# Optimization experiments

Measured on AMD Instinct MI355X. Metric: run time of the kernel, lower is better.

Reference implementation:

```python
import jax, jax.numpy as jnp
import numpy as np
from jax import lax

N_G, E_G, E_LG = 100000, 400000, 1200000
N_T, E_T, E_LGT = 50000, 100000, 300000
D_F, D_MSG_G = 64, 128
VOCAB, D_EMB, D_MSG_T = 780, 128, 128
N_ITERS_G, N_ITERS_T = 4, 4
SCALE = 0.05  # keep relu/sum chains numerically tame over iterations


def setup_inputs() -> dict:
    key = jax.random.key(0)
    ks = jax.random.split(key, 32)
    f32 = jnp.float32
    w = lambda k, sh: jax.random.normal(k, sh, f32) * SCALE
    return {
        "G_f": jax.random.normal(ks[0], (N_G, D_F), f32),
        "G_ef": jax.random.normal(ks[1], (E_G, D_F), f32),
        "G_src": jax.random.randint(ks[2], (E_G,), 0, N_G, jnp.int32),
        "G_dst": jax.random.randint(ks[3], (E_G,), 0, N_G, jnp.int32),
        "G_lg_src": jax.random.randint(ks[4], (E_LG,), 0, E_G, jnp.int32),
        "G_lg_dst": jax.random.randint(ks[5], (E_LG,), 0, E_G, jnp.int32),
        "T_id": jax.random.randint(ks[6], (N_T,), 0, VOCAB, jnp.int32),
        "T_src": jax.random.randint(ks[7], (E_T,), 0, N_T, jnp.int32),
        "T_dst": jax.random.randint(ks[8], (E_T,), 0, N_T, jnp.int32),
        "T_lg_src": jax.random.randint(ks[9], (E_LGT,), 0, E_T, jnp.int32),
        "T_lg_dst": jax.random.randint(ks[10], (E_LGT,), 0, E_T, jnp.int32),
        "embeddings": jax.random.normal(ks[11], (VOCAB, D_EMB), f32),
        "W1": w(ks[12], (D_F, D_MSG_G)),
        "W2": w(ks[13], (D_F, D_MSG_G)),
        "W3": w(ks[14], (D_MSG_G, D_MSG_G)),
        "U1_G": w(ks[15], (D_F, D_MSG_G)),
        "U2_G": w(ks[16], (D_MSG_G, D_MSG_G)),
        "Wz": w(ks[17], (D_EMB, D_MSG_T)),
        "Uz": w(ks[18], (D_MSG_T, D_MSG_T)),
        "Wr": w(ks[19], (D_EMB, D_MSG_T)),
        "Ur": w(ks[20], (D_MSG_T, D_MSG_T)),
        "Wh": w(ks[21], (D_EMB, D_MSG_T)),
        "Uh": w(ks[22], (D_MSG_T, D_MSG_T)),
        "U1_T": w(ks[23], (D_EMB, D_MSG_T)),
        "U2_T": w(ks[24], (D_MSG_T, D_MSG_T)),
    }


def reference(G_f, G_ef, G_src, G_dst, G_lg_src, G_lg_dst,
              T_id, T_src, T_dst, T_lg_src, T_lg_dst,
              embeddings, W1, W2, W3, U1_G, U2_G,
              Wz, Uz, Wr, Ur, Wh, Uh, U1_T, U2_T):
    seg = jax.ops.segment_sum

    # ---- molecule graph G: loopy-BP MLP messages on the line graph ----
    f_src_G = G_f[G_src]                               # [E_G, D_F] copy_src
    base_G = f_src_G @ W1 + G_ef @ W2                  # loop-invariant part of g1_G

    def stepG(msg, _):
        sum_msg = seg(msg[G_lg_src], G_lg_dst, num_segments=E_G)
        return jax.nn.relu(base_G + sum_msg @ W3), None

    msgG0 = jnp.zeros((E_G, D_MSG_G), G_f.dtype)
    msgG, _ = lax.scan(stepG, msgG0, None, length=N_ITERS_G)

    # readout g2_G: sum edge msgs into dst nodes
    sG = seg(msgG, G_dst, num_segments=N_G)
    x_G = jax.nn.relu(G_f @ U1_G + sG @ U2_G)          # [N_G, D_MSG_G]

    # ---- junction tree T: GRU messages on the tree line graph ----
    f_T = embeddings[T_id]                             # one-hot id @ embeddings
    f_src_T = f_T[T_src]                               # [E_T, D_EMB]
    xz, xr, xh = f_src_T @ Wz, f_src_T @ Wr, f_src_T @ Wh

    def stepT(msg, _):
        s = seg(msg[T_lg_src], T_lg_dst, num_segments=E_T)
        z = jax.nn.sigmoid(xz + s @ Uz)
        r = jax.nn.sigmoid(xr + s @ Ur)
        h = jnp.tanh(xh + (r * s) @ Uh)
        return (1.0 - z) * s + z * h, None

    msgT0 = jnp.zeros((E_T, D_MSG_T), f_T.dtype)
    msgT, _ = lax.scan(stepT, msgT0, None, length=N_ITERS_T)

    sT = seg(msgT, T_dst, num_segments=N_T)
    x_T = jax.nn.relu(f_T @ U1_T + sT @ U2_T)          # [N_T, D_MSG_T]

    # concat node readouts (same width) so output is a single array
    return jnp.concatenate([x_G, x_T], axis=0)         # [N_G+N_T, 128]
```

## Files before the change

kernel.cpp:

```cpp
#include <hip/hip_runtime.h>

#define NG 100000
#define EG 400000
#define ELG 1200000
#define NT 50000
#define ET 100000
#define ELGT 300000

#define GEG ((EG + 63) / 64)
#define GET ((ET + 63) / 64)
#define GNG ((NG + 63) / 64)
#define GNT ((NT + 63) / 64)

#define SEG1 EG
#define SEG2 (EG + NG)
#define SEG3 (EG + NG + ET)
#define NSEG_ALL (EG + NG + ET + NT)
#define NE_ALL (ELG + EG + ELGT + ET)
#define NE_PAD (NE_ALL + 3 * NSEG_ALL + 64)

typedef unsigned short u16;
typedef unsigned int u32;
typedef __attribute__((ext_vector_type(8))) short bf16x8;
typedef __attribute__((ext_vector_type(4))) float f32x4;
typedef __attribute__((ext_vector_type(4))) u32 u32x4;
typedef __attribute__((ext_vector_type(2))) u32 u32x2;

#define TILE_B 16384

__device__ __forceinline__ float bflo(u32 p){ return __uint_as_float(p << 16); }
__device__ __forceinline__ float bfhi(u32 p){ return __uint_as_float(p & 0xffff0000u); }
__device__ __forceinline__ float bf2f(u16 h){ return __uint_as_float(((u32)h) << 16); }
__device__ __forceinline__ u16 f2bf(float f){
  u32 u = __float_as_uint(f);
  u32 r = u + 0x7fffu + ((u >> 16) & 1u);
  return (u16)(r >> 16);
}
__device__ __forceinline__ float sigm(float x){ return 1.0f / (1.0f + __expf(-x)); }
__device__ __forceinline__ float tanh_(float x){ return 2.0f / (1.0f + __expf(-2.0f * x)) - 1.0f; }
__device__ __forceinline__ float relu_(float x){ return x > 0.0f ? x : 0.0f; }
__device__ __forceinline__ void wfence(){ __builtin_amdgcn_wave_barrier(); }

__device__ __forceinline__ uint4 ldnt4(const void* p){
  u32x4 v = __builtin_nontemporal_load((const u32x4*)p);
  return make_uint4(v.x, v.y, v.z, v.w);
}
__device__ __forceinline__ void stnt4(void* p, uint4 d){
  u32x4 v = {d.x, d.y, d.z, d.w};
  __builtin_nontemporal_store(v, (u32x4*)p);
}
__device__ __forceinline__ uint2 ldnt2(const void* p){
  u32x2 v = __builtin_nontemporal_load((const u32x2*)p);
  return make_uint2(v.x, v.y);
}
__device__ __forceinline__ void stnt2(void* p, uint2 d){
  u32x2 v = {d.x, d.y};
  __builtin_nontemporal_store(v, (u32x2*)p);
}

__device__ __forceinline__ int swz(int r, int c){ return r * 256 + (c ^ ((r & 7) << 4)); }

__device__ __forceinline__ void zero8(float v[8]){
  #pragma unroll
  for (int j = 0; j < 8; j++) v[j] = 0.f;
}
__device__ __forceinline__ uint4 pack8(const float v[8]){
  uint4 o;
  o.x = f2bf(v[0]) | ((u32)f2bf(v[1]) << 16);
  o.y = f2bf(v[2]) | ((u32)f2bf(v[3]) << 16);
  o.z = f2bf(v[4]) | ((u32)f2bf(v[5]) << 16);
  o.w = f2bf(v[6]) | ((u32)f2bf(v[7]) << 16);
  return o;
}
__device__ __forceinline__ uint2 pack4(const f32x4& a){
  uint2 o;
  o.x = (u32)f2bf(a[0]) | ((u32)f2bf(a[1]) << 16);
  o.y = (u32)f2bf(a[2]) | ((u32)f2bf(a[3]) << 16);
  return o;
}
__device__ __forceinline__ void unp4(uint2 u, float v[4]){
  v[0] = bflo(u.x); v[1] = bfhi(u.x); v[2] = bflo(u.y); v[3] = bfhi(u.y);
}
__device__ __forceinline__ bf16x8 packfrag(const float v[8]){
  union { uint4 u; bf16x8 b; } c; c.u = pack8(v); return c.b;
}
__device__ __forceinline__ bf16x8 zfrag(){
  union { uint4 u; bf16x8 b; } c; c.u = make_uint4(0, 0, 0, 0); return c.b;
}
__device__ __forceinline__ bf16x8 as_frag(uint4 u){
  union { uint4 u; bf16x8 b; } c; c.u = u; return c.b;
}

__global__ void k_sniff(const u32* __restrict__ g, int* __restrict__ flag){
  __shared__ int sh[2];
  if (threadIdx.x < 2) sh[threadIdx.x] = 0;
  __syncthreads();
  int c0 = 0, c1 = 0;
  for (int i = 0; i < 16; i++){
    u32 w = g[threadIdx.x * 16 + i];
    u32 lo = w & 0xFFFFu;
    if (lo == 0u) c0++;
    else { u32 e = (lo >> 7) & 0xFFu; if (e >= 96u && e <= 144u) c1++; }
  }
  atomicAdd(&sh[0], c0); atomicAdd(&sh[1], c1);
  __syncthreads();
  if (threadIdx.x == 0) *flag = (sh[0] < 512 && sh[1] > 2048) ? 1 : 0;
}

__global__ void k_cvt_all(const void* p0, const void* p1, const void* p2, const void* p3,
                          const void* p4, const void* p5, const void* p6, const void* p7,
                          const void* p8, const void* p9, const void* p10, const void* p11,
                          const void* p12, float* __restrict__ wm, const int* __restrict__ flagp){
  int i = blockIdx.x * 256 + threadIdx.x;
  if (i >= 188416) return;
  const int offs[14] = {0,8192,16384,32768,40960,57344,73728,90112,106496,122880,139264,155648,172032,188416};
  const void* ps[13] = {p0,p1,p2,p3,p4,p5,p6,p7,p8,p9,p10,p11,p12};
  int w = 0;
  while (i >= offs[w + 1]) w++;
  int li = i - offs[w];
  wm[i] = (*flagp) ? bf2f(((const u16*)ps[w])[li]) : ((const float*)ps[w])[li];
}

__global__ void k_mkfrag_all(const float* __restrict__ wm, u16* __restrict__ frag){
  const int wmo[13] = {0,8192,16384,32768,40960,57344,73728,90112,106496,122880,139264,155648,172032};
  const int nks[13] = {2,2,4,2,4,4,4,4,4,4,4,4,4};
  int b = blockIdx.x;
  int wi = 0, ks = b;
  while (ks >= nks[wi]){ ks -= nks[wi]; wi++; }
  const float* W = wm + wmo[wi];
  int nt = threadIdx.x >> 6, lane = threadIdx.x & 63;
  int kr = ks * 32 + ((lane >> 4) << 3);
  int col = nt * 16 + (lane & 15);
  u16* o = frag + (size_t)b * 4096 + nt * 512 + lane * 8;
  #pragma unroll
  for (int j = 0; j < 8; j++) o[j] = f2bf(W[(size_t)(kr + j) * 128 + col]);
}

__device__ __forceinline__ const void* rowdt(const void* mat, size_t row, int W, int bf){
  return bf ? (const void*)((const u16*)mat + row * (size_t)W)
            : (const void*)((const float*)mat + row * (size_t)W);
}
__device__ __forceinline__ void load8(const void* rowbase, int c8, int bf, float v[8]){
  if (bf){
    uint4 d = ((const uint4*)rowbase)[c8];
    v[0]=bflo(d.x); v[1]=bfhi(d.x); v[2]=bflo(d.y); v[3]=bfhi(d.y);
    v[4]=bflo(d.z); v[5]=bfhi(d.z); v[6]=bflo(d.w); v[7]=bfhi(d.w);
  } else {
    const float4* p = (const float4*)rowbase + (c8 << 1);
    float4 a = p[0], b = p[1];
    v[0]=a.x; v[1]=a.y; v[2]=a.z; v[3]=a.w; v[4]=b.x; v[5]=b.y; v[6]=b.z; v[7]=b.w;
  }
}
__device__ __forceinline__ void load8_nt(const void* rowbase, int c8, int bf, float v[8]){
  if (bf){
    uint4 d = ldnt4((const uint4*)rowbase + c8);
    v[0]=bflo(d.x); v[1]=bfhi(d.x); v[2]=bflo(d.y); v[3]=bfhi(d.y);
    v[4]=bflo(d.z); v[5]=bfhi(d.z); v[6]=bflo(d.w); v[7]=bfhi(d.w);
  } else {
    uint4 a = ldnt4((const float4*)rowbase + (c8 << 1));
    uint4 b = ldnt4((const float4*)rowbase + (c8 << 1) + 1);
    v[0]=__uint_as_float(a.x); v[1]=__uint_as_float(a.y);
    v[2]=__uint_as_float(a.z); v[3]=__uint_as_float(a.w);
    v[4]=__uint_as_float(b.x); v[5]=__uint_as_float(b.y);
    v[6]=__uint_as_float(b.z); v[7]=__uint_as_float(b.w);
  }
}

__global__ void k_hist_all(const int* __restrict__ Glgd, const int* __restrict__ Gd,
                           const int* __restrict__ Tlgd, const int* __restrict__ Td,
                           int* __restrict__ cnt){
  int e = blockIdx.x * 256 + threadIdx.x;
  if (e >= NE_ALL) return;
  int seg;
  if (e < ELG)                       seg = Glgd[e];
  else if (e < ELG + EG)             seg = SEG1 + Gd[e - ELG];
  else if (e < ELG + EG + ELGT)      seg = SEG2 + Tlgd[e - ELG - EG];
  else                               seg = SEG3 + Td[e - ELG - EG - ELGT];
  atomicAdd(&cnt[seg], 1);
}

__global__ void k_scan1(const int* __restrict__ cnt, int n, int* __restrict__ csum){
  int base = blockIdx.x * 4096, tid = threadIdx.x;
  int s = 0;
  for (int i = 0; i < 16; i++){
    int idx = base + i * 256 + tid;
    if (idx < n) s += (cnt[idx] + 3) & ~3;
  }
  __shared__ int red[4];
  for (int off = 32; off; off >>= 1) s += __shfl_down(s, off, 64);
  if ((tid & 63) == 0) red[tid >> 6] = s;
  __syncthreads();
  if (tid == 0) csum[blockIdx.x] = red[0] + red[1] + red[2] + red[3];
}

__global__ void k_scan2(int* csum, int nch, int* rowptr, int n){
  if (threadIdx.x == 0){
    int run = 0;
    for (int c = 0; c < nch; c++){ int t = csum[c]; csum[c] = run; run += t; }
    rowptr[n] = run;
  }
}

__global__ void k_scan3(const int* __restrict__ cnt, int n, const int* __restrict__ csum,
                        int* __restrict__ rowptr){
  __shared__ int buf[4096];
  __shared__ int tsum[256];
  int base = blockIdx.x * 4096, tid = threadIdx.x;
  for (int i = 0; i < 16; i++){
    int idx = base + i * 256 + tid;
    buf[i * 256 + tid] = (idx < n) ? ((cnt[idx] + 3) & ~3) : 0;
  }
  __syncthreads();
  int run = 0;
  for (int i = 0; i < 16; i++){ int v = buf[tid * 16 + i]; buf[tid * 16 + i] = run; run += v; }
  tsum[tid] = run;
  __syncthreads();
  for (int off = 1; off < 256; off <<= 1){
    int v = (tid >= off) ? tsum[tid - off] : 0;
    __syncthreads();
    tsum[tid] += v;
    __syncthreads();
  }
  int texcl = tsum[tid] - run;
  int cbase = csum[blockIdx.x];
  for (int i = 0; i < 16; i++){
    int idx = base + tid * 16 + i;
    if (idx < n) rowptr[idx] = cbase + texcl + buf[tid * 16 + i];
  }
}

__global__ void k_fill_all(const int* __restrict__ Glgd, const int* __restrict__ Glgs,
                           const int* __restrict__ Gd,
                           const int* __restrict__ Tlgd, const int* __restrict__ Tlgs,
                           const int* __restrict__ Td,
                           const int* __restrict__ rowptr, int* __restrict__ fill,
                           int* __restrict__ col){
  int e = blockIdx.x * 256 + threadIdx.x;
  if (e >= NE_ALL) return;
  int seg, srcv;
  if (e < ELG){                      seg = Glgd[e];                           srcv = Glgs[e]; }
  else if (e < ELG + EG){            int l = e - ELG;                         seg = SEG1 + Gd[l];   srcv = l; }
  else if (e < ELG + EG + ELGT){     int l = e - ELG - EG;                    seg = SEG2 + Tlgd[l]; srcv = Tlgs[l]; }
  else {                             int l = e - ELG - EG - ELGT;             seg = SEG3 + Td[l];   srcv = l; }
  int pos = atomicAdd(&fill[seg], 1);
  col[rowptr[seg] + pos] = srcv;
}

__global__ void k_fill_pad(const int* __restrict__ cnt, const int* __restrict__ rowptr,
                           int* __restrict__ col){
  int seg = blockIdx.x * 256 + threadIdx.x;
  if (seg >= NSEG_ALL) return;
  int dummy = (seg < SEG2) ? EG : ET;
  int start = rowptr[seg] + cnt[seg];
  int end = rowptr[seg + 1];
  for (int q = start; q < end; q++) col[q] = dummy;
}

__global__ void k_zero_dummy(u16* a, u16* b, u16* c, u16* d){
  int i = threadIdx.x;
  if (i < 128){
    a[(size_t)EG * 128 + i] = 0; b[(size_t)EG * 128 + i] = 0;
    c[(size_t)ET * 128 + i] = 0; d[(size_t)ET * 128 + i] = 0;
  }
}


__device__ __forceinline__ void acc8_add(float (&a)[8], uint4 d){
  a[0] += bflo(d.x); a[1] += bfhi(d.x);
  a[2] += bflo(d.y); a[3] += bfhi(d.y);
  a[4] += bflo(d.z); a[5] += bfhi(d.z);
  a[6] += bflo(d.w); a[7] += bfhi(d.w);
}

__device__ __forceinline__ void gather_accum(const int* __restrict__ rowptr,
    const int* __restrict__ colidx, const u16* __restrict__ msg,
    int row, int M, int kg, float (&acc)[4][8])
{
  #pragma unroll
  for (int ks = 0; ks < 4; ks++) zero8(acc[ks]);
  if (row >= M) return;
  int p = rowptr[row], pe = rowptr[row + 1];
  for (; p < pe; p += 4){
    uint4 ci = *(const uint4*)(colidx + p);
    const uint4* b0 = (const uint4*)(msg + (size_t)ci.x * 128);
    const uint4* b1 = (const uint4*)(msg + (size_t)ci.y * 128);
    const uint4* b2 = (const uint4*)(msg + (size_t)ci.z * 128);
    const uint4* b3 = (const uint4*)(msg + (size_t)ci.w * 128);
    uint4 v0[4], v1[4], v2[4], v3[4];
    #pragma unroll
    for (int ks = 0; ks < 4; ks++){
      v0[ks] = b0[ks * 4 + kg]; v1[ks] = b1[ks * 4 + kg];
      v2[ks] = b2[ks * 4 + kg]; v3[ks] = b3[ks * 4 + kg];
    }
    #pragma unroll
    for (int ks = 0; ks < 4; ks++){
      acc8_add(acc[ks], v0[ks]); acc8_add(acc[ks], v1[ks]);
      acc8_add(acc[ks], v2[ks]); acc8_add(acc[ks], v3[ks]);
    }
  }
}

template<int KS>
__device__ __forceinline__ void mma_f(const bf16x8* a, const u16* __restrict__ frag,
                                      f32x4 (&acc)[8])
{
  int lane = threadIdx.x & 63;
  #pragma unroll
  for (int ks = 0; ks < KS; ks++){
    const u16* fb = frag + (size_t)ks * 4096 + lane * 8;
    #pragma unroll
    for (int nt = 0; nt < 8; nt++){
      bf16x8 b = *(const bf16x8*)(fb + (size_t)nt * 512);
      acc[nt] = __builtin_amdgcn_mfma_f32_16x16x32_bf16(a[ks], b, acc[nt], 0, 0, 0);
    }
  }
}

#define INIT_ACC(A) { _Pragma("unroll") for (int n_=0;n_<8;n_++){ A[n_][0]=0.f; A[n_][1]=0.f; A[n_][2]=0.f; A[n_][3]=0.f; } }

__device__ __forceinline__ void repack_store(const char* __restrict__ tile,
    u16* __restrict__ dst, int row0, int M)
{
  int rl = threadIdx.x >> 2, q = threadIdx.x & 3;
  int grow = row0 + rl;
  if (grow < M){
    #pragma unroll
    for (int v = 0; v < 4; v++){
      uint4 d = *(const uint4*)(tile + swz(rl, (v * 4 + q) * 16));
      stnt4(dst + (size_t)grow * 128 + (size_t)(v * 4 + q) * 8, d);
    }
  }
}

__device__ __forceinline__ size_t fslot(int blk, int w, int nt){
  return ((((size_t)blk * 4 + w) * 8 + nt) * 64 + (threadIdx.x & 63)) * 4;
}

__device__ __forceinline__ void load_catfrag(const void* __restrict__ Gf,
    const void* __restrict__ Gef, const int* __restrict__ Gsrc,
    int arow, int kg, int bf, bf16x8 (&fC)[4])
{
  if (arow < EG){
    int sr = Gsrc[arow];
    const void* ra = rowdt(Gf, (size_t)sr, 64, bf);
    const void* rb = rowdt(Gef, (size_t)arow, 64, bf);
    float t[8];
    load8(ra, kg, bf, t);        fC[0] = packfrag(t);
    load8(ra, 4 + kg, bf, t);    fC[1] = packfrag(t);
    load8_nt(rb, kg, bf, t);     fC[2] = packfrag(t);
    load8_nt(rb, 4 + kg, bf, t); fC[3] = packfrag(t);
  } else {
    #pragma unroll
    for (int ks = 0; ks < 4; ks++) fC[ks] = zfrag();
  }
}


__global__ __launch_bounds__(256, 4) void k_init(
    const void* __restrict__ Gf, const void* __restrict__ Gef, const int* __restrict__ Gsrc,
    const u16* __restrict__ fWcat, const int* __restrict__ flagp, u16* __restrict__ msgG,
    const void* __restrict__ emb, const int* __restrict__ Tid, const int* __restrict__ Tsrc,
    const u16* __restrict__ fWz, const u16* __restrict__ fWr, const u16* __restrict__ fWh,
    u16* __restrict__ xzf, u16* __restrict__ xrf, u16* __restrict__ xhf, u16* __restrict__ msgT)
{
  __shared__ char t0[TILE_B];
  int bf = *flagp;
  int lane = threadIdx.x & 63, w = threadIdx.x >> 6;
  int stripe = w * 16, kg = lane >> 4, m16 = lane & 15;
  if (blockIdx.x < GET){
    int blk = blockIdx.x, row0 = blk * 64, arow = row0 + stripe + m16;
    bf16x8 fE[4];
    if (arow < ET){
      int id = Tid[Tsrc[arow]];
      const void* rb = rowdt(emb, (size_t)id, 128, bf);
      #pragma unroll
      for (int ks = 0; ks < 4; ks++){
        float t[8]; load8(rb, ks * 4 + kg, bf, t); fE[ks] = packfrag(t);
      }
    } else {
      #pragma unroll
      for (int ks = 0; ks < 4; ks++) fE[ks] = zfrag();
    }
    f32x4 acc[8];
    uint2 zpk[8];
    INIT_ACC(acc);
    mma_f<4>(fE, fWz, acc);
    #pragma unroll
    for (int nt = 0; nt < 8; nt++){
      zpk[nt] = pack4(acc[nt]);
      stnt2(xzf + fslot(blk, w, nt), zpk[nt]);
    }
    INIT_ACC(acc);
    mma_f<4>(fE, fWr, acc);
    #pragma unroll
    for (int nt = 0; nt < 8; nt++)
      stnt2(xrf + fslot(blk, w, nt), pack4(acc[nt]));
    INIT_ACC(acc);
    mma_f<4>(fE, fWh, acc);
    #pragma unroll
    for (int nt = 0; nt < 8; nt++){
      stnt2(xhf + fslot(blk, w, nt), pack4(acc[nt]));
      float xzv[4]; unp4(zpk[nt], xzv);
      #pragma unroll
      for (int r = 0; r < 4; r++){
        int rt = stripe + (kg << 2) + r;
        int cb = nt * 32 + m16 * 2;
        *(u16*)(t0 + swz(rt, cb)) = f2bf(sigm(xzv[r]) * tanh_(acc[nt][r]));
      }
    }
    wfence();
    repack_store(t0, msgT, row0, ET);
  } else {
    int blk = blockIdx.x - GET, row0 = blk * 64, arow = row0 + stripe + m16;
    bf16x8 fC[4];
    load_catfrag(Gf, Gef, Gsrc, arow, kg, bf, fC);
    f32x4 acc[8]; INIT_ACC(acc);
    mma_f<4>(fC, fWcat, acc);
    #pragma unroll
    for (int nt = 0; nt < 8; nt++)
      #pragma unroll
      for (int r = 0; r < 4; r++){
        int rt = stripe + (kg << 2) + r;
        int cb = nt * 32 + m16 * 2;
        *(u16*)(t0 + swz(rt, cb)) = f2bf(relu_(acc[nt][r]));
      }
    wfence();
    repack_store(t0, msgG, row0, EG);
  }
}

__global__ __launch_bounds__(256, 4) void k_iter(
    const u16* __restrict__ msgInG, u16* __restrict__ msgOutG,
    const void* __restrict__ Gf, const void* __restrict__ Gef, const int* __restrict__ Gsrc,
    const int* __restrict__ rp, const int* __restrict__ col,
    const u16* __restrict__ fWcat, const u16* __restrict__ fW3, const int* __restrict__ flagp,
    const u16* __restrict__ msgInT, u16* __restrict__ msgOutT,
    const u16* __restrict__ fUz, const u16* __restrict__ fUr, const u16* __restrict__ fUh,
    const u16* __restrict__ xzf, const u16* __restrict__ xrf, const u16* __restrict__ xhf)
{
  __shared__ char t0[TILE_B];
  __shared__ char t1[TILE_B];
  int lane = threadIdx.x & 63, w = threadIdx.x >> 6;
  int stripe = w * 16, kg = lane >> 4, m16 = lane & 15;
  if (blockIdx.x < GET){
    int blk = blockIdx.x, row0 = blk * 64, arow = row0 + stripe + m16;
    float ga[4][8];
    gather_accum(rp + SEG2, col, msgInT, arow, ET, kg, ga);
    bf16x8 fS[4];
    #pragma unroll
    for (int ks = 0; ks < 4; ks++){
      uint4 pk = pack8(ga[ks]);
      *(uint4*)(t0 + swz(stripe + m16, ks * 64 + kg * 16)) = pk;
      fS[ks] = as_frag(pk);
    }
    f32x4 acc[8];
    INIT_ACC(acc);
    mma_f<4>(fS, fUr, acc);
    wfence();
    #pragma unroll
    for (int nt = 0; nt < 8; nt++){
      uint2 r4 = ldnt2(xrf + fslot(blk, w, nt));
      float xrv[4]; unp4(r4, xrv);
      #pragma unroll
      for (int r = 0; r < 4; r++){
        int rt = stripe + (kg << 2) + r;
        int cb = nt * 32 + m16 * 2;
        float s = bf2f(*(const u16*)(t0 + swz(rt, cb)));
        float rr = sigm(xrv[r] + acc[nt][r]);
        *(u16*)(t1 + swz(rt, cb)) = f2bf(rr * s);
      }
    }
    wfence();
    bf16x8 fRS[4];
    #pragma unroll
    for (int ks = 0; ks < 4; ks++)
      fRS[ks] = *(const bf16x8*)(t1 + swz(stripe + m16, ks * 64 + kg * 16));
    INIT_ACC(acc);
    mma_f<4>(fRS, fUh, acc);
    wfence();
    #pragma unroll
    for (int nt = 0; nt < 8; nt++){
      uint2 h4 = ldnt2(xhf + fslot(blk, w, nt));
      float xhv[4]; unp4(h4, xhv);
      #pragma unroll
      for (int r = 0; r < 4; r++){
        int rt = stripe + (kg << 2) + r;
        int cb = nt * 32 + m16 * 2;
        *(u16*)(t1 + swz(rt, cb)) = f2bf(tanh_(xhv[r] + acc[nt][r]));
      }
    }
    wfence();
    bf16x8 fS2[4];
    #pragma unroll
    for (int ks = 0; ks < 4; ks++)
      fS2[ks] = *(const bf16x8*)(t0 + swz(stripe + m16, ks * 64 + kg * 16));
    INIT_ACC(acc);
    mma_f<4>(fS2, fUz, acc);
    wfence();
    #pragma unroll
    for (int nt = 0; nt < 8; nt++){
      uint2 z4 = ldnt2(xzf + fslot(blk, w, nt));
      float xzv[4]; unp4(z4, xzv);
      #pragma unroll
      for (int r = 0; r < 4; r++){
        int rt = stripe + (kg << 2) + r;
        int cb = nt * 32 + m16 * 2;
        float z = sigm(xzv[r] + acc[nt][r]);
        float s = bf2f(*(const u16*)(t0 + swz(rt, cb)));
        float h = bf2f(*(const u16*)(t1 + swz(rt, cb)));
        *(u16*)(t0 + swz(rt, cb)) = f2bf((1.f - z) * s + z * h);
      }
    }
    wfence();
    repack_store(t0, msgOutT, row0, ET);
  } else {
    int bf = *flagp;
    int blk = blockIdx.x - GET, row0 = blk * 64, arow = row0 + stripe + m16;
    float ga[4][8];
    gather_accum(rp, col, msgInG, arow, EG, kg, ga);
    bf16x8 fS[4];
    #pragma unroll
    for (int ks = 0; ks < 4; ks++) fS[ks] = packfrag(ga[ks]);
    bf16x8 fC[4];
    load_catfrag(Gf, Gef, Gsrc, arow, kg, bf, fC);
    f32x4 acc[8]; INIT_ACC(acc);
    mma_f<4>(fS, fW3, acc);
    mma_f<4>(fC, fWcat, acc);
    #pragma unroll
    for (int nt = 0; nt < 8; nt++)
      #pragma unroll
      for (int r = 0; r < 4; r++){
        int rt = stripe + (kg << 2) + r;
        int cb = nt * 32 + m16 * 2;
        *(u16*)(t0 + swz(rt, cb)) = f2bf(relu_(acc[nt][r]));
      }
    wfence();
    repack_store(t0, msgOutG, row0, EG);
  }
}

__global__ __launch_bounds__(256, 4) void k_readout(
    const void* __restrict__ Gf, const u16* __restrict__ msgG,
    const int* __restrict__ rp, const int* __restrict__ col,
    const u16* __restrict__ fU1G, const u16* __restrict__ fU2G,
    const void* __restrict__ emb, const int* __restrict__ Tid, const u16* __restrict__ msgT,
    const u16* __restrict__ fU1T, const u16* __restrict__ fU2T,
    const int* __restrict__ flagp, float* __restrict__ out)
{
  int bf = *flagp;
  int lane = threadIdx.x & 63, w = threadIdx.x >> 6;
  int stripe = w * 16, kg = lane >> 4, m16 = lane & 15;
  if (blockIdx.x < GNT){
    int row0 = blockIdx.x * 64, arow = row0 + stripe + m16;
    float ga[4][8];
    gather_accum(rp + SEG3, col, msgT, arow, NT, kg, ga);
    bf16x8 fS[4];
    #pragma unroll
    for (int ks = 0; ks < 4; ks++) fS[ks] = packfrag(ga[ks]);
    bf16x8 fE[4];
    if (arow < NT){
      int id = Tid[arow];
      const void* rb = rowdt(emb, (size_t)id, 128, bf);
      #pragma unroll
      for (int ks = 0; ks < 4; ks++){
        float t[8]; load8(rb, ks * 4 + kg, bf, t); fE[ks] = packfrag(t);
      }
    } else {
      #pragma unroll
      for (int ks = 0; ks < 4; ks++) fE[ks] = zfrag();
    }
    f32x4 acc[8]; INIT_ACC(acc);
    mma_f<4>(fS, fU2T, acc);
    mma_f<4>(fE, fU1T, acc);
    #pragma unroll
    for (int nt = 0; nt < 8; nt++)
      #pragma unroll
      for (int r = 0; r < 4; r++){
        int R = row0 + stripe + (kg << 2) + r;
        if (R < NT) __builtin_nontemporal_store(relu_(acc[nt][r]),
                        &out[(size_t)(NG + R) * 128 + nt * 16 + m16]);
      }
  } else {
    int row0 = (blockIdx.x - GNT) * 64, arow = row0 + stripe + m16;
    float ga[4][8];
    gather_accum(rp + SEG1, col, msgG, arow, NG, kg, ga);
    bf16x8 fS[4];
    #pragma unroll
    for (int ks = 0; ks < 4; ks++) fS[ks] = packfrag(ga[ks]);
    bf16x8 fG[2];
    if (arow < NG){
      const void* ra = rowdt(Gf, (size_t)arow, 64, bf);
      float t[8];
      load8_nt(ra, kg, bf, t);     fG[0] = packfrag(t);
      load8_nt(ra, 4 + kg, bf, t); fG[1] = packfrag(t);
    } else { fG[0] = zfrag(); fG[1] = zfrag(); }
    f32x4 acc[8]; INIT_ACC(acc);
    mma_f<4>(fS, fU2G, acc);
    mma_f<2>(fG, fU1G, acc);
    #pragma unroll
    for (int nt = 0; nt < 8; nt++)
      #pragma unroll
      for (int r = 0; r < 4; r++){
        int R = row0 + stripe + (kg << 2) + r;
        if (R < NG) __builtin_nontemporal_store(relu_(acc[nt][r]),
                        &out[(size_t)R * 128 + nt * 16 + m16]);
      }
  }
}

extern "C" void kernel_launch(void* const* d_in, const int* in_sizes, int n_in,
                              void* d_out, int out_size, void* d_ws, size_t ws_size,
                              hipStream_t stream)
{
  const void* G_f      = d_in[0];
  const void* G_ef     = d_in[1];
  const int*  G_src    = (const int*)d_in[2];
  const int*  G_dst    = (const int*)d_in[3];
  const int*  G_lg_src = (const int*)d_in[4];
  const int*  G_lg_dst = (const int*)d_in[5];
  const int*  T_id     = (const int*)d_in[6];
  const int*  T_src    = (const int*)d_in[7];
  const int*  T_dst    = (const int*)d_in[8];
  const int*  T_lg_src = (const int*)d_in[9];
  const int*  T_lg_dst = (const int*)d_in[10];
  const void* emb      = d_in[11];
  float* out = (float*)d_out;
  (void)in_sizes; (void)n_in; (void)out_size; (void)ws_size;

  size_t off = 0;
  auto alloc = [&](size_t bytes) -> char* {
    char* p = (char*)d_ws + off;
    off += (bytes + 255) & ~(size_t)255;
    return p;
  };

  int*   flag = (int*)alloc(256);
  float* wm   = (float*)alloc(sizeof(float) * 188416);
  u16*   frag = (u16*)alloc(2 * 46 * 4096);
  const u16* fWcat = frag;
  const u16* fW3   = frag + (size_t)4  * 4096;
  const u16* fU1G  = frag + (size_t)8  * 4096;
  const u16* fU2G  = frag + (size_t)10 * 4096;
  const u16* fWz   = frag + (size_t)14 * 4096;
  const u16* fUz   = frag + (size_t)18 * 4096;
  const u16* fWr   = frag + (size_t)22 * 4096;
  const u16* fUr   = frag + (size_t)26 * 4096;
  const u16* fWh   = frag + (size_t)30 * 4096;
  const u16* fUh   = frag + (size_t)34 * 4096;
  const u16* fU1T  = frag + (size_t)38 * 4096;
  const u16* fU2T  = frag + (size_t)42 * 4096;

  int* rp   = (int*)alloc(sizeof(int) * (NSEG_ALL + 1));
  int* col  = (int*)alloc(sizeof(int) * NE_PAD);
  int* cnt  = (int*)alloc(sizeof(int) * 2 * NSEG_ALL);
  int* csum = (int*)alloc(sizeof(int) * 256);
  u16* msgGA = (u16*)alloc((size_t)(EG + 1) * 128 * 2);
  u16* msgGB = (u16*)alloc((size_t)(EG + 1) * 128 * 2);
  u16* xzf   = (u16*)alloc((size_t)GET * 8192 * 2);
  u16* xrf   = (u16*)alloc((size_t)GET * 8192 * 2);
  u16* xhf   = (u16*)alloc((size_t)GET * 8192 * 2);
  u16* msgTA = (u16*)alloc((size_t)(ET + 1) * 128 * 2);
  u16* msgTB = (u16*)alloc((size_t)(ET + 1) * 128 * 2);

  k_sniff<<<1, 256, 0, stream>>>((const u32*)G_ef, flag);
  k_cvt_all<<<(188416 + 255) / 256, 256, 0, stream>>>(
      d_in[12], d_in[13], d_in[14], d_in[15], d_in[16], d_in[17], d_in[18],
      d_in[19], d_in[20], d_in[21], d_in[22], d_in[23], d_in[24], wm, flag);
  k_mkfrag_all<<<46, 512, 0, stream>>>(wm, frag);
  k_zero_dummy<<<1, 128, 0, stream>>>(msgGA, msgGB, msgTA, msgTB);

  hipMemsetAsync(cnt, 0, sizeof(int) * 2 * NSEG_ALL, stream);
  k_hist_all<<<(NE_ALL + 255) / 256, 256, 0, stream>>>(G_lg_dst, G_dst, T_lg_dst, T_dst, cnt);
  int nch = (NSEG_ALL + 4095) / 4096;
  k_scan1<<<nch, 256, 0, stream>>>(cnt, NSEG_ALL, csum);
  k_scan2<<<1, 64, 0, stream>>>(csum, nch, rp, NSEG_ALL);
  k_scan3<<<nch, 256, 0, stream>>>(cnt, NSEG_ALL, csum, rp);
  k_fill_all<<<(NE_ALL + 255) / 256, 256, 0, stream>>>(
      G_lg_dst, G_lg_src, G_dst, T_lg_dst, T_lg_src, T_dst, rp, cnt + NSEG_ALL, col);
  k_fill_pad<<<(NSEG_ALL + 255) / 256, 256, 0, stream>>>(cnt, rp, col);

  k_init<<<GET + GEG, 256, 0, stream>>>(G_f, G_ef, G_src, fWcat, flag, msgGA,
                                        emb, T_id, T_src, fWz, fWr, fWh, xzf, xrf, xhf, msgTA);
  k_iter<<<GET + GEG, 256, 0, stream>>>(msgGA, msgGB, G_f, G_ef, G_src, rp, col, fWcat, fW3, flag,
                                        msgTA, msgTB, fUz, fUr, fUh, xzf, xrf, xhf);
  k_iter<<<GET + GEG, 256, 0, stream>>>(msgGB, msgGA, G_f, G_ef, G_src, rp, col, fWcat, fW3, flag,
                                        msgTB, msgTA, fUz, fUr, fUh, xzf, xrf, xhf);
  k_iter<<<GET + GEG, 256, 0, stream>>>(msgGA, msgGB, G_f, G_ef, G_src, rp, col, fWcat, fW3, flag,
                                        msgTA, msgTB, fUz, fUr, fUh, xzf, xrf, xhf);
  k_readout<<<GNT + GNG, 256, 0, stream>>>(G_f, msgGB, rp, col, fU1G, fU2G,
                                           emb, T_id, msgTB, fU1T, fU2T, flag, out);
}
```

Before: 1.102 ms.

## Merge setup and fill/init kernels to cut launches and overlap independent stages

Weight conversion, fragment packing, dummy-row zeroing and the edge histogram now run as one block-partitioned setup kernel. Fragments are built straight from the raw weights, which removes the intermediate fp32 buffer and one pass over it. The CSR fill, padding and the message-init GEMM blocks now share one launch, so fill atomics can overlap with the init tensor work. This cuts several launch gaps, at the cost of larger heterogeneous kernels whose block-role dispatch and shared-memory reservation also apply to the light blocks.

Result: no change. 1.094 ms (-0.7%).

```diff
diff --git a/kernel.cpp b/kernel.cpp
--- a/kernel.cpp
+++ b/kernel.cpp
@@ -18,6 +18,10 @@
 #define NSEG_ALL (EG + NG + ET + NT)
 #define NE_ALL (ELG + EG + ELGT + ET)
 #define NE_PAD (NE_ALL + 3 * NSEG_ALL + 64)
+
+#define HISTB ((NE_ALL + 511) / 512)
+#define FILLB ((NE_ALL + 255) / 256)
+#define PADB  ((NSEG_ALL + 255) / 256)
 
 typedef unsigned short u16;
 typedef unsigned int u32;
@@ -107,35 +111,9 @@
   if (threadIdx.x == 0) *flag = (sh[0] < 512 && sh[1] > 2048) ? 1 : 0;
 }
 
-__global__ void k_cvt_all(const void* p0, const void* p1, const void* p2, const void* p3,
-                          const void* p4, const void* p5, const void* p6, const void* p7,
-                          const void* p8, const void* p9, const void* p10, const void* p11,
-                          const void* p12, float* __restrict__ wm, const int* __restrict__ flagp){
-  int i = blockIdx.x * 256 + threadIdx.x;
-  if (i >= 188416) return;
-  const int offs[14] = {0,8192,16384,32768,40960,57344,73728,90112,106496,122880,139264,155648,172032,188416};
-  const void* ps[13] = {p0,p1,p2,p3,p4,p5,p6,p7,p8,p9,p10,p11,p12};
-  int w = 0;
-  while (i >= offs[w + 1]) w++;
-  int li = i - offs[w];
-  wm[i] = (*flagp) ? bf2f(((const u16*)ps[w])[li]) : ((const float*)ps[w])[li];
-}
-
-__global__ void k_mkfrag_all(const float* __restrict__ wm, u16* __restrict__ frag){
-  const int wmo[13] = {0,8192,16384,32768,40960,57344,73728,90112,106496,122880,139264,155648,172032};
-  const int nks[13] = {2,2,4,2,4,4,4,4,4,4,4,4,4};
-  int b = blockIdx.x;
-  int wi = 0, ks = b;
-  while (ks >= nks[wi]){ ks -= nks[wi]; wi++; }
-  const float* W = wm + wmo[wi];
-  int nt = threadIdx.x >> 6, lane = threadIdx.x & 63;
-  int kr = ks * 32 + ((lane >> 4) << 3);
-  int col = nt * 16 + (lane & 15);
-  u16* o = frag + (size_t)b * 4096 + nt * 512 + lane * 8;
-  #pragma unroll
-  for (int j = 0; j < 8; j++) o[j] = f2bf(W[(size_t)(kr + j) * 128 + col]);
-}
-
+__device__ __forceinline__ float eldt(const void* mat, size_t idx, int bf){
+  return bf ? bf2f(((const u16*)mat)[idx]) : ((const float*)mat)[idx];
+}
 __device__ __forceinline__ const void* rowdt(const void* mat, size_t row, int W, int bf){
   return bf ? (const void*)((const u16*)mat + row * (size_t)W)
             : (const void*)((const float*)mat + row * (size_t)W);
@@ -166,17 +144,47 @@
   }
 }
 
-__global__ void k_hist_all(const int* __restrict__ Glgd, const int* __restrict__ Gd,
-                           const int* __restrict__ Tlgd, const int* __restrict__ Td,
-                           int* __restrict__ cnt){
-  int e = blockIdx.x * 256 + threadIdx.x;
-  if (e >= NE_ALL) return;
-  int seg;
-  if (e < ELG)                       seg = Glgd[e];
-  else if (e < ELG + EG)             seg = SEG1 + Gd[e - ELG];
-  else if (e < ELG + EG + ELGT)      seg = SEG2 + Tlgd[e - ELG - EG];
-  else                               seg = SEG3 + Td[e - ELG - EG - ELGT];
-  atomicAdd(&cnt[seg], 1);
+__global__ __launch_bounds__(512) void k_setup(
+    const void* p0, const void* p1, const void* p2, const void* p3, const void* p4,
+    const void* p5, const void* p6, const void* p7, const void* p8, const void* p9,
+    const void* p10, const void* p11, const void* p12,
+    u16* __restrict__ frag, const int* __restrict__ flagp,
+    u16* __restrict__ mA, u16* __restrict__ mB, u16* __restrict__ mC, u16* __restrict__ mD,
+    const int* __restrict__ Glgd, const int* __restrict__ Gd,
+    const int* __restrict__ Tlgd, const int* __restrict__ Td,
+    int* __restrict__ cnt)
+{
+  int b = blockIdx.x;
+  if (b < 46){
+    const int nks[13] = {2,2,4,2,4,4,4,4,4,4,4,4,4};
+    const void* ps[13] = {p0,p1,p2,p3,p4,p5,p6,p7,p8,p9,p10,p11,p12};
+    int bf = *flagp;
+    int wi = 0, ks = b;
+    while (ks >= nks[wi]){ ks -= nks[wi]; wi++; }
+    const void* W = ps[wi];
+    int nt = threadIdx.x >> 6, lane = threadIdx.x & 63;
+    int kr = ks * 32 + ((lane >> 4) << 3);
+    int col = nt * 16 + (lane & 15);
+    u16* o = frag + (size_t)b * 4096 + nt * 512 + lane * 8;
+    #pragma unroll
+    for (int j = 0; j < 8; j++)
+      o[j] = f2bf(eldt(W, (size_t)(kr + j) * 128 + col, bf));
+  } else if (b == 46){
+    int i = threadIdx.x;
+    if (i < 128){
+      mA[(size_t)EG * 128 + i] = 0; mB[(size_t)EG * 128 + i] = 0;
+      mC[(size_t)ET * 128 + i] = 0; mD[(size_t)ET * 128 + i] = 0;
+    }
+  } else {
+    int e = (b - 47) * 512 + threadIdx.x;
+    if (e >= NE_ALL) return;
+    int seg;
+    if (e < ELG)                       seg = Glgd[e];
+    else if (e < ELG + EG)             seg = SEG1 + Gd[e - ELG];
+    else if (e < ELG + EG + ELGT)      seg = SEG2 + Tlgd[e - ELG - EG];
+    else                               seg = SEG3 + Td[e - ELG - EG - ELGT];
+    atomicAdd(&cnt[seg], 1);
+  }
 }
 
 __global__ void k_scan1(const int* __restrict__ cnt, int n, int* __restrict__ csum){
@@ -226,41 +234,6 @@
   for (int i = 0; i < 16; i++){
     int idx = base + tid * 16 + i;
     if (idx < n) rowptr[idx] = cbase + texcl + buf[tid * 16 + i];
-  }
-}
-
-__global__ void k_fill_all(const int* __restrict__ Glgd, const int* __restrict__ Glgs,
-                           const int* __restrict__ Gd,
-                           const int* __restrict__ Tlgd, const int* __restrict__ Tlgs,
-                           const int* __restrict__ Td,
-                           const int* __restrict__ rowptr, int* __restrict__ fill,
-                           int* __restrict__ col){
-  int e = blockIdx.x * 256 + threadIdx.x;
-  if (e >= NE_ALL) return;
-  int seg, srcv;
-  if (e < ELG){                      seg = Glgd[e];                           srcv = Glgs[e]; }
-  else if (e < ELG + EG){            int l = e - ELG;                         seg = SEG1 + Gd[l];   srcv = l; }
-  else if (e < ELG + EG + ELGT){     int l = e - ELG - EG;                    seg = SEG2 + Tlgd[l]; srcv = Tlgs[l]; }
-  else {                             int l = e - ELG - EG - ELGT;             seg = SEG3 + Td[l];   srcv = l; }
-  int pos = atomicAdd(&fill[seg], 1);
-  col[rowptr[seg] + pos] = srcv;
-}
-
-__global__ void k_fill_pad(const int* __restrict__ cnt, const int* __restrict__ rowptr,
-                           int* __restrict__ col){
-  int seg = blockIdx.x * 256 + threadIdx.x;
-  if (seg >= NSEG_ALL) return;
-  int dummy = (seg < SEG2) ? EG : ET;
-  int start = rowptr[seg] + cnt[seg];
-  int end = rowptr[seg + 1];
-  for (int q = start; q < end; q++) col[q] = dummy;
-}
-
-__global__ void k_zero_dummy(u16* a, u16* b, u16* c, u16* d){
-  int i = threadIdx.x;
-  if (i < 128){
-    a[(size_t)EG * 128 + i] = 0; b[(size_t)EG * 128 + i] = 0;
-    c[(size_t)ET * 128 + i] = 0; d[(size_t)ET * 128 + i] = 0;
   }
 }
 
@@ -355,8 +328,83 @@
   }
 }
 
-
-__global__ __launch_bounds__(256, 4) void k_init(
+__device__ __forceinline__ void init_body(int idx,
+    const void* __restrict__ Gf, const void* __restrict__ Gef, const int* __restrict__ Gsrc,
+    const u16* __restrict__ fWcat, int bf, u16* __restrict__ msgG,
+    const void* __restrict__ emb, const int* __restrict__ Tid, const int* __restrict__ Tsrc,
+    const u16* __restrict__ fWz, const u16* __restrict__ fWr, const u16* __restrict__ fWh,
+    u16* __restrict__ xzf, u16* __restrict__ xrf, u16* __restrict__ xhf, u16* __restrict__ msgT,
+    char* t0)
+{
+  int lane = threadIdx.x & 63, w = threadIdx.x >> 6;
+  int stripe = w * 16, kg = lane >> 4, m16 = lane & 15;
+  if (idx < GET){
+    int blk = idx, row0 = blk * 64, arow = row0 + stripe + m16;
+    bf16x8 fE[4];
+    if (arow < ET){
+      int id = Tid[Tsrc[arow]];
+      const void* rb = rowdt(emb, (size_t)id, 128, bf);
+      #pragma unroll
+      for (int ks = 0; ks < 4; ks++){
+        float t[8]; load8(rb, ks * 4 + kg, bf, t); fE[ks] = packfrag(t);
+      }
+    } else {
+      #pragma unroll
+      for (int ks = 0; ks < 4; ks++) fE[ks] = zfrag();
+    }
+    f32x4 acc[8];
+    uint2 zpk[8];
+    INIT_ACC(acc);
+    mma_f<4>(fE, fWz, acc);
+    #pragma unroll
+    for (int nt = 0; nt < 8; nt++){
+      zpk[nt] = pack4(acc[nt]);
+      stnt2(xzf + fslot(blk, w, nt), zpk[nt]);
+    }
+    INIT_ACC(acc);
+    mma_f<4>(fE, fWr, acc);
+    #pragma unroll
+    for (int nt = 0; nt < 8; nt++)
+      stnt2(xrf + fslot(blk, w, nt), pack4(acc[nt]));
+    INIT_ACC(acc);
+    mma_f<4>(fE, fWh, acc);
+    #pragma unroll
+    for (int nt = 0; nt < 8; nt++){
+      stnt2(xhf + fslot(blk, w, nt), pack4(acc[nt]));
+      float xzv[4]; unp4(zpk[nt], xzv);
+      #pragma unroll
+      for (int r = 0; r < 4; r++){
+        int rt = stripe + (kg << 2) + r;
+        int cb = nt * 32 + m16 * 2;
+        *(u16*)(t0 + swz(rt, cb)) = f2bf(sigm(xzv[r]) * tanh_(acc[nt][r]));
+      }
+    }
+    wfence();
+    repack_store(t0, msgT, row0, ET);
+  } else {
+    int blk = idx - GET, row0 = blk * 64, arow = row0 + stripe + m16;
+    bf16x8 fC[4];
+    load_catfrag(Gf, Gef, Gsrc, arow, kg, bf, fC);
+    f32x4 acc[8]; INIT_ACC(acc);
+    mma_f<4>(fC, fWcat, acc);
+    #pragma unroll
+    for (int nt = 0; nt < 8; nt++)
+      #pragma unroll
+      for (int r = 0; r < 4; r++){
+        int rt = stripe + (kg << 2) + r;
+        int cb = nt * 32 + m16 * 2;
+        *(u16*)(t0 + swz(rt, cb)) = f2bf(relu_(acc[nt][r]));
+      }
+    wfence();
+    repack_store(t0, msgG, row0, EG);
+  }
+}
+
+__global__ __launch_bounds__(256, 4) void k_fill_init(
+    const int* __restrict__ Glgd, const int* __restrict__ Glgs, const int* __restrict__ Gd,
+    const int* __restrict__ Tlgd, const int* __restrict__ Tlgs, const int* __restrict__ Td,
+    const int* __restrict__ rowptr, int* __restrict__ fill, int* __restrict__ col,
+    const int* __restrict__ cnt,
     const void* __restrict__ Gf, const void* __restrict__ Gef, const int* __restrict__ Gsrc,
     const u16* __restrict__ fWcat, const int* __restrict__ flagp, u16* __restrict__ msgG,
     const void* __restrict__ emb, const int* __restrict__ Tid, const int* __restrict__ Tsrc,
@@ -364,68 +412,27 @@
     u16* __restrict__ xzf, u16* __restrict__ xrf, u16* __restrict__ xhf, u16* __restrict__ msgT)
 {
   __shared__ char t0[TILE_B];
-  int bf = *flagp;
-  int lane = threadIdx.x & 63, w = threadIdx.x >> 6;
-  int stripe = w * 16, kg = lane >> 4, m16 = lane & 15;
-  if (blockIdx.x < GET){
-    int blk = blockIdx.x, row0 = blk * 64, arow = row0 + stripe + m16;
-    bf16x8 fE[4];
-    if (arow < ET){
-      int id = Tid[Tsrc[arow]];
-      const void* rb = rowdt(emb, (size_t)id, 128, bf);
-      #pragma unroll
-      for (int ks = 0; ks < 4; ks++){
-        float t[8]; load8(rb, ks * 4 + kg, bf, t); fE[ks] = packfrag(t);
-      }
-    } else {
-      #pragma unroll
-      for (int ks = 0; ks < 4; ks++) fE[ks] = zfrag();
-    }
-    f32x4 acc[8];
-    uint2 zpk[8];
-    INIT_ACC(acc);
-    mma_f<4>(fE, fWz, acc);
-    #pragma unroll
-    for (int nt = 0; nt < 8; nt++){
-      zpk[nt] = pack4(acc[nt]);
-      stnt2(xzf + fslot(blk, w, nt), zpk[nt]);
-    }
-    INIT_ACC(acc);
-    mma_f<4>(fE, fWr, acc);
-    #pragma unroll
-    for (int nt = 0; nt < 8; nt++)
-      stnt2(xrf + fslot(blk, w, nt), pack4(acc[nt]));
-    INIT_ACC(acc);
-    mma_f<4>(fE, fWh, acc);
-    #pragma unroll
-    for (int nt = 0; nt < 8; nt++){
-      stnt2(xhf + fslot(blk, w, nt), pack4(acc[nt]));
-      float xzv[4]; unp4(zpk[nt], xzv);
-      #pragma unroll
-      for (int r = 0; r < 4; r++){
-        int rt = stripe + (kg << 2) + r;
-        int cb = nt * 32 + m16 * 2;
-        *(u16*)(t0 + swz(rt, cb)) = f2bf(sigm(xzv[r]) * tanh_(acc[nt][r]));
-      }
-    }
-    wfence();
-    repack_store(t0, msgT, row0, ET);
-  } else {
-    int blk = blockIdx.x - GET, row0 = blk * 64, arow = row0 + stripe + m16;
-    bf16x8 fC[4];
-    load_catfrag(Gf, Gef, Gsrc, arow, kg, bf, fC);
-    f32x4 acc[8]; INIT_ACC(acc);
-    mma_f<4>(fC, fWcat, acc);
-    #pragma unroll
-    for (int nt = 0; nt < 8; nt++)
-      #pragma unroll
-      for (int r = 0; r < 4; r++){
-        int rt = stripe + (kg << 2) + r;
-        int cb = nt * 32 + m16 * 2;
-        *(u16*)(t0 + swz(rt, cb)) = f2bf(relu_(acc[nt][r]));
-      }
-    wfence();
-    repack_store(t0, msgG, row0, EG);
+  int b = blockIdx.x;
+  if (b < FILLB){
+    int e = b * 256 + threadIdx.x;
+    if (e >= NE_ALL) return;
+    int seg, srcv;
+    if (e < ELG){                      seg = Glgd[e];                           srcv = Glgs[e]; }
+    else if (e < ELG + EG){            int l = e - ELG;                         seg = SEG1 + Gd[l];   srcv = l; }
+    else if (e < ELG + EG + ELGT){     int l = e - ELG - EG;                    seg = SEG2 + Tlgd[l]; srcv = Tlgs[l]; }
+    else {                             int l = e - ELG - EG - ELGT;             seg = SEG3 + Td[l];   srcv = l; }
+    int pos = atomicAdd(&fill[seg], 1);
+    col[rowptr[seg] + pos] = srcv;
+  } else if (b < FILLB + PADB){
+    int seg = (b - FILLB) * 256 + threadIdx.x;
+    if (seg >= NSEG_ALL) return;
+    int dummy = (seg < SEG2) ? EG : ET;
+    int start = rowptr[seg] + cnt[seg];
+    int end = rowptr[seg + 1];
+    for (int q = start; q < end; q++) col[q] = dummy;
+  } else {
+    init_body(b - FILLB - PADB, Gf, Gef, Gsrc, fWcat, *flagp, msgG,
+              emb, Tid, Tsrc, fWz, fWr, fWh, xzf, xrf, xhf, msgT, t0);
   }
 }
 
@@ -635,7 +642,6 @@
   };
 
   int*   flag = (int*)alloc(256);
-  float* wm   = (float*)alloc(sizeof(float) * 188416);
   u16*   frag = (u16*)alloc(2 * 46 * 4096);
   const u16* fWcat = frag;
   const u16* fW3   = frag + (size_t)4  * 4096;
@@ -662,25 +668,25 @@
   u16* msgTA = (u16*)alloc((size_t)(ET + 1) * 128 * 2);
   u16* msgTB = (u16*)alloc((size_t)(ET + 1) * 128 * 2);
 
+  hipMemsetAsync(cnt, 0, sizeof(int) * 2 * NSEG_ALL, stream);
   k_sniff<<<1, 256, 0, stream>>>((const u32*)G_ef, flag);
-  k_cvt_all<<<(188416 + 255) / 256, 256, 0, stream>>>(
+  k_setup<<<47 + HISTB, 512, 0, stream>>>(
       d_in[12], d_in[13], d_in[14], d_in[15], d_in[16], d_in[17], d_in[18],
-      d_in[19], d_in[20], d_in[21], d_in[22], d_in[23], d_in[24], wm, flag);
-  k_mkfrag_all<<<46, 512, 0, stream>>>(wm, frag);
-  k_zero_dummy<<<1, 128, 0, stream>>>(msgGA, msgGB, msgTA, msgTB);
-
-  hipMemsetAsync(cnt, 0, sizeof(int) * 2 * NSEG_ALL, stream);
-  k_hist_all<<<(NE_ALL + 255) / 256, 256, 0, stream>>>(G_lg_dst, G_dst, T_lg_dst, T_dst, cnt);
+      d_in[19], d_in[20], d_in[21], d_in[22], d_in[23], d_in[24],
+      frag, flag, msgGA, msgGB, msgTA, msgTB,
+      G_lg_dst, G_dst, T_lg_dst, T_dst, cnt);
+
   int nch = (NSEG_ALL + 4095) / 4096;
   k_scan1<<<nch, 256, 0, stream>>>(cnt, NSEG_ALL, csum);
   k_scan2<<<1, 64, 0, stream>>>(csum, nch, rp, NSEG_ALL);
   k_scan3<<<nch, 256, 0, stream>>>(cnt, NSEG_ALL, csum, rp);
-  k_fill_all<<<(NE_ALL + 255) / 256, 256, 0, stream>>>(
-      G_lg_dst, G_lg_src, G_dst, T_lg_dst, T_lg_src, T_dst, rp, cnt + NSEG_ALL, col);
-  k_fill_pad<<<(NSEG_ALL + 255) / 256, 256, 0, stream>>>(cnt, rp, col);
-
-  k_init<<<GET + GEG, 256, 0, stream>>>(G_f, G_ef, G_src, fWcat, flag, msgGA,
-                                        emb, T_id, T_src, fWz, fWr, fWh, xzf, xrf, xhf, msgTA);
+
+  k_fill_init<<<FILLB + PADB + GET + GEG, 256, 0, stream>>>(
+      G_lg_dst, G_lg_src, G_dst, T_lg_dst, T_lg_src, T_dst,
+      rp, cnt + NSEG_ALL, col, cnt,
+      G_f, G_ef, G_src, fWcat, flag, msgGA,
+      emb, T_id, T_src, fWz, fWr, fWh, xzf, xrf, xhf, msgTA);
+
   k_iter<<<GET + GEG, 256, 0, stream>>>(msgGA, msgGB, G_f, G_ef, G_src, rp, col, fWcat, fW3, flag,
                                         msgTA, msgTB, fUz, fUr, fUh, xzf, xrf, xhf);
   k_iter<<<GET + GEG, 256, 0, stream>>>(msgGB, msgGA, G_f, G_ef, G_src, rp, col, fWcat, fW3, flag,
```
